# Optimization experiments

Measured on AMD Instinct MI355X. Metric: run time of the kernel, lower is better.

## Reference

```python
import jax, jax.numpy as jnp
import numpy as np

N, E, IN_DIM, OUT_DIM, R = 100000, 1600000, 128, 128, 8


def setup_inputs() -> dict:
    key = jax.random.key(0)
    k = jax.random.split(key, 6)
    scale_rel = np.sqrt(6.0 / (IN_DIM + OUT_DIM))  # xavier_uniform bound
    x = jax.random.normal(k[0], (N, IN_DIM), dtype=jnp.float32)
    edge_index = jax.random.randint(k[1], (2, E), 0, N, dtype=jnp.int64)
    edge_type = jax.random.randint(k[2], (E,), 0, R, dtype=jnp.int64)
    rel_weight = jax.random.uniform(k[3], (R, IN_DIM, OUT_DIM), dtype=jnp.float32,
                                    minval=-scale_rel, maxval=scale_rel)
    w_self = jax.random.uniform(k[4], (IN_DIM, OUT_DIM), dtype=jnp.float32,
                                minval=-scale_rel, maxval=scale_rel)
    b_self = jax.random.normal(k[5], (OUT_DIM,), dtype=jnp.float32) * 0.01
    return {"x": x, "edge_index": edge_index, "edge_type": edge_type,
            "rel_weight": rel_weight, "w_self": w_self, "b_self": b_self}


def reference(x, edge_index, edge_type, rel_weight, w_self, b_self):
    n = x.shape[0]
    src, dst = edge_index[0], edge_index[1]
    # self-loop term: W_self @ h_v + b
    out = x @ w_self + b_self                                  # (N, out)
    # pre-transform every node by every relation, then gather per edge.
    # equivalent to per-relation masked (x[src_r] @ W_r) + scatter_add.
    xw = jnp.einsum('ni,rio->nro', x, rel_weight)               # (N, R, out)
    msg = xw[src, edge_type]                                    # (E, out)
    agg = jax.ops.segment_sum(msg, dst, num_segments=n)         # (N, out)
    deg = jax.ops.segment_sum(jnp.ones(dst.shape[0], x.dtype), dst, num_segments=n)
    deg = jnp.clip(deg, 1.0)[:, None]                           # (N, 1)
    return jax.nn.relu(out + agg / deg)
```

## Files before the change

### kernel.cpp

```cpp
#include <hip/hip_runtime.h>
#include <hip/hip_bf16.h>

typedef __attribute__((ext_vector_type(4))) float f32x4_t;
typedef __attribute__((ext_vector_type(8))) short bf16x8_t;

__device__ __forceinline__ float bf2f(ushort u) {
  return __uint_as_float(((unsigned)u) << 16);
}
__device__ __forceinline__ ushort f2bf(float f) {
  unsigned u = __float_as_uint(f);
  u += 0x7fffu + ((u >> 16) & 1u);
  return (ushort)(u >> 16);
}

__global__ void deg_kernel(const int* __restrict__ dst, int* __restrict__ deg, long E) {
  long i = (long)blockIdx.x * blockDim.x + threadIdx.x;
  long st = (long)gridDim.x * blockDim.x;
  for (; i < E; i += st) atomicAdd(&deg[dst[i]], 1);
}

__global__ __launch_bounds__(256) void scan1(const int* __restrict__ deg, int* __restrict__ starts,
                                             int* __restrict__ bsum, int N) {
  __shared__ int lds[256];
  const int tid = threadIdx.x;
  const int base = blockIdx.x * 1024 + tid * 4;
  int v0 = 0, v1 = 0, v2 = 0, v3 = 0;
  if (base + 3 < N) {
    int4 q = *(const int4*)(deg + base);
    v0 = q.x; v1 = q.y; v2 = q.z; v3 = q.w;
  } else {
    if (base + 0 < N) v0 = deg[base];
    if (base + 1 < N) v1 = deg[base + 1];
    if (base + 2 < N) v2 = deg[base + 2];
    if (base + 3 < N) v3 = deg[base + 3];
  }
  int s = v0 + v1 + v2 + v3;
  lds[tid] = s;
  __syncthreads();
  for (int off = 1; off < 256; off <<= 1) {
    int t = (tid >= off) ? lds[tid - off] : 0;
    __syncthreads();
    lds[tid] += t;
    __syncthreads();
  }
  int p = lds[tid] - s;
  if (tid == 255) bsum[blockIdx.x] = lds[255];
  if (base + 0 < N) starts[base + 0] = p; p += v0;
  if (base + 1 < N) starts[base + 1] = p; p += v1;
  if (base + 2 < N) starts[base + 2] = p; p += v2;
  if (base + 3 < N) starts[base + 3] = p;
}

__global__ void scan2(int* __restrict__ bsum, int nb) {
  if (threadIdx.x == 0 && blockIdx.x == 0) {
    int acc = 0;
    for (int i = 0; i < nb; i++) { int t = bsum[i]; bsum[i] = acc; acc += t; }
  }
}

__global__ void scan3(int* __restrict__ starts, int* __restrict__ cursor,
                      const int* __restrict__ bsum, int N) {
  int i = blockIdx.x * 256 + threadIdx.x;
  if (i < N) {
    int v = starts[i] + bsum[i >> 10];
    starts[i] = v;
    cursor[i] = v;
  }
}

__global__ void fill_csr(const int* __restrict__ src, const int* __restrict__ dst,
                         const int* __restrict__ et, int* __restrict__ cursor,
                         uint* __restrict__ packed, long E) {
  long i = (long)blockIdx.x * blockDim.x + threadIdx.x;
  long st = (long)gridDim.x * blockDim.x;
  for (; i < E; i += st) {
    int pos = atomicAdd(&cursor[dst[i]], 1);
    packed[pos] = ((uint)src[i] << 4) | (uint)et[i];
  }
}

__global__ void build_wT(const float* __restrict__ rel, const float* __restrict__ wself,
                         ushort* __restrict__ wT, int R) {
  int id = blockIdx.x * blockDim.x + threadIdx.x;
  int total = (R + 1) * 128 * 128;
  if (id >= total) return;
  int r = id >> 14;
  int rem = id & 16383;
  int o = rem >> 7;
  int i = rem & 127;
  float v = (r < R) ? rel[((size_t)r << 14) + (i << 7) + o] : wself[(i << 7) + o];
  wT[id] = f2bf(v);
}

__global__ __launch_bounds__(512) void xw_gemm(const float* __restrict__ x,
                                               const ushort* __restrict__ wT,
                                               ushort* __restrict__ xw,
                                               int N, int NR) {
  __shared__ ushort smem[2][16384];

  const int tid = threadIdx.x;
  const int lane = tid & 63;
  const int wave = tid >> 6;
  const int l15 = lane & 15;
  const int l4 = lane >> 4;
  const int nodebase = blockIdx.x * 256 + wave * 32;

  bf16x8_t xf[2][4];
  int nd[2];
#pragma unroll
  for (int g = 0; g < 2; g++) {
    int node = nodebase + g * 16 + l15;
    nd[g] = node;
    int ra = (node < N) ? node : (N - 1);
    const float* xrow = x + (size_t)ra * 128 + l4 * 8;
#pragma unroll
    for (int kk = 0; kk < 4; kk++) {
      float4 v0 = *(const float4*)(xrow + kk * 32);
      float4 v1 = *(const float4*)(xrow + kk * 32 + 4);
      bf16x8_t t;
      t[0] = (short)f2bf(v0.x); t[1] = (short)f2bf(v0.y);
      t[2] = (short)f2bf(v0.z); t[3] = (short)f2bf(v0.w);
      t[4] = (short)f2bf(v1.x); t[5] = (short)f2bf(v1.y);
      t[6] = (short)f2bf(v1.z); t[7] = (short)f2bf(v1.w);
      xf[g][kk] = t;
    }
  }

  {
    bf16x8_t sreg[4];
#pragma unroll
    for (int j = 0; j < 4; j++) {
      int c = tid + j * 512;
      sreg[j] = *(const bf16x8_t*)(wT + c * 8);
    }
#pragma unroll
    for (int j = 0; j < 4; j++) {
      int c = tid + j * 512;
      int o = c >> 4;
      int colb = (c & 15) * 16;
      int byte = o * 256 + (colb ^ ((o & 7) << 4));
      *(bf16x8_t*)((char*)smem[0] + byte) = sreg[j];
    }
  }
  __syncthreads();

  for (int r = 0; r < NR; r++) {
    bf16x8_t sreg[4];
    const bool pf = (r + 1 < NR);
    if (pf) {
      const ushort* wsrc = wT + ((size_t)(r + 1) << 14);
#pragma unroll
      for (int j = 0; j < 4; j++) {
        int c = tid + j * 512;
        sreg[j] = *(const bf16x8_t*)(wsrc + c * 8);
      }
    }

    const char* wbuf = (const char*)smem[r & 1];
#pragma unroll
    for (int nt = 0; nt < 8; nt++) {
      bf16x8_t wf[4];
      const int row = nt * 16 + l15;
      const int swz = (row & 7) << 4;
#pragma unroll
      for (int kk = 0; kk < 4; kk++) {
        int colb = l4 * 16 + kk * 64;
        wf[kk] = *(const bf16x8_t*)(wbuf + row * 256 + (colb ^ swz));
      }
#pragma unroll
      for (int g = 0; g < 2; g++) {
        f32x4_t acc = {0.f, 0.f, 0.f, 0.f};
#pragma unroll
        for (int kk = 0; kk < 4; kk++)
          acc = __builtin_amdgcn_mfma_f32_16x16x32_bf16(wf[kk], xf[g][kk], acc, 0, 0, 0);
        if (nd[g] < N) {
          ushort4 pk;
          pk.x = f2bf(acc[0]); pk.y = f2bf(acc[1]);
          pk.z = f2bf(acc[2]); pk.w = f2bf(acc[3]);
          *(ushort4*)(xw + ((size_t)nd[g] * NR + r) * 128 + nt * 16 + l4 * 4) = pk;
        }
      }
    }

    if (pf) {
#pragma unroll
      for (int j = 0; j < 4; j++) {
        int c = tid + j * 512;
        int o = c >> 4;
        int colb = (c & 15) * 16;
        int byte = o * 256 + (colb ^ ((o & 7) << 4));
        *(bf16x8_t*)((char*)smem[(r + 1) & 1] + byte) = sreg[j];
      }
    }
    __syncthreads();
  }
}

__global__ __launch_bounds__(256) void gather_out(const ushort* __restrict__ xw,
                                                  const uint* __restrict__ packed,
                                                  const int* __restrict__ starts,
                                                  const int* __restrict__ deg,
                                                  const float* __restrict__ b,
                                                  float* __restrict__ out,
                                                  int N, int NR, int R) {
  const int lane = threadIdx.x & 63;
  const int d = blockIdx.x * 4 + (threadIdx.x >> 6);
  if (d >= N) return;
  const int s0 = starts[d];
  const int dg = deg[d];
  const int e1 = s0 + dg;
  float a0 = 0.f, a1 = 0.f;
  int e = s0;
  for (; e + 1 < e1; e += 2) {
    uint r0 = packed[e], r1 = packed[e + 1];
    ushort2 m0 = *(const ushort2*)(xw + ((size_t)(r0 >> 4) * NR + (r0 & 15u)) * 128 + lane * 2);
    ushort2 m1 = *(const ushort2*)(xw + ((size_t)(r1 >> 4) * NR + (r1 & 15u)) * 128 + lane * 2);
    a0 += bf2f(m0.x) + bf2f(m1.x);
    a1 += bf2f(m0.y) + bf2f(m1.y);
  }
  if (e < e1) {
    uint r0 = packed[e];
    ushort2 m0 = *(const ushort2*)(xw + ((size_t)(r0 >> 4) * NR + (r0 & 15u)) * 128 + lane * 2);
    a0 += bf2f(m0.x);
    a1 += bf2f(m0.y);
  }
  float inv = 1.0f / (float)((dg > 1) ? dg : 1);
  ushort2 sf = *(const ushort2*)(xw + ((size_t)d * NR + R) * 128 + lane * 2);
  float2 bb = ((const float2*)b)[lane];
  float* op = out + (size_t)d * 128 + lane * 2;
  op[0] = fmaxf(bf2f(sf.x) + bb.x + a0 * inv, 0.f);
  op[1] = fmaxf(bf2f(sf.y) + bb.y + a1 * inv, 0.f);
}

__global__ void naive_edge(const float* __restrict__ x, const int* __restrict__ src,
                           const int* __restrict__ dst, const int* __restrict__ et,
                           const float* __restrict__ rel, float* __restrict__ agg, long E) {
  const int lane = threadIdx.x & 63;
  long wid = ((long)blockIdx.x * blockDim.x + threadIdx.x) >> 6;
  long nw = ((long)gridDim.x * blockDim.x) >> 6;
  for (long e = wid; e < E; e += nw) {
    int s = src[e];
    int d = dst[e];
    int t = et[e];
    const float* xs = x + (size_t)s * 128;
    const float* w = rel + (size_t)t * 128 * 128;
    float a0 = 0.f, a1 = 0.f;
    for (int i = 0; i < 128; i++) {
      float xv = xs[i];
      a0 += xv * w[i * 128 + lane];
      a1 += xv * w[i * 128 + lane + 64];
    }
    atomicAdd(agg + (size_t)d * 128 + lane, a0);
    atomicAdd(agg + (size_t)d * 128 + lane + 64, a1);
  }
}
__global__ void naive_self(const float* __restrict__ x, const float* __restrict__ ws,
                           const float* __restrict__ b, const int* __restrict__ deg,
                           float* __restrict__ out, int N) {
  int v = blockIdx.x;
  int o = threadIdx.x;
  if (v >= N) return;
  const float* xv = x + (size_t)v * 128;
  float acc = b[o];
  for (int i = 0; i < 128; i++) acc += xv[i] * ws[i * 128 + o];
  float dg = (float)max(deg[v], 1);
  float val = acc + out[(size_t)v * 128 + o] / dg;
  out[(size_t)v * 128 + o] = fmaxf(val, 0.f);
}

extern "C" void kernel_launch(void* const* d_in, const int* in_sizes, int n_in,
                              void* d_out, int out_size, void* d_ws, size_t ws_size,
                              hipStream_t stream) {
  const float* x = (const float*)d_in[0];
  const int* ei = (const int*)d_in[1];
  const int* et = (const int*)d_in[2];
  const float* rel = (const float*)d_in[3];
  const float* wself = (const float*)d_in[4];
  const float* bself = (const float*)d_in[5];
  float* out = (float*)d_out;

  const int N = in_sizes[0] / 128;
  const long E = in_sizes[2];
  const int R = in_sizes[3] / (128 * 128);
  const int NR = R + 1;
  const int* srcp = ei;
  const int* dstp = ei + E;

  size_t off = 0;
  auto alloc = [&](size_t bytes) {
    size_t o = off;
    off += (bytes + 255) & ~(size_t)255;
    return o;
  };
  size_t deg_off = alloc((size_t)N * 4);
  size_t starts_off = alloc((size_t)N * 4);
  size_t cursor_off = alloc((size_t)N * 4);
  size_t bsum_off = alloc(4096);
  size_t wT_off = alloc((size_t)NR * 128 * 128 * 2);
  size_t packed_off = alloc((size_t)E * 4);
  size_t xw_off = alloc((size_t)N * (size_t)NR * 128 * 2);
  const bool main_path = (ws_size >= off);

  int* deg = (int*)((char*)d_ws + deg_off);
  hipMemsetAsync(deg, 0, (size_t)N * 4, stream);
  deg_kernel<<<2048, 256, 0, stream>>>(dstp, deg, E);

  if (main_path) {
    int* starts = (int*)((char*)d_ws + starts_off);
    int* cursor = (int*)((char*)d_ws + cursor_off);
    int* bsum = (int*)((char*)d_ws + bsum_off);
    ushort* wT = (ushort*)((char*)d_ws + wT_off);
    uint* packed = (uint*)((char*)d_ws + packed_off);
    ushort* xw = (ushort*)((char*)d_ws + xw_off);

    const int nb = (N + 1023) / 1024;
    scan1<<<nb, 256, 0, stream>>>(deg, starts, bsum, N);
    scan2<<<1, 64, 0, stream>>>(bsum, nb);
    scan3<<<(N + 255) / 256, 256, 0, stream>>>(starts, cursor, bsum, N);
    fill_csr<<<2048, 256, 0, stream>>>(srcp, dstp, et, cursor, packed, E);
    build_wT<<<(NR * 16384 + 255) / 256, 256, 0, stream>>>(rel, wself, wT, R);
    xw_gemm<<<(N + 255) / 256, 512, 0, stream>>>(x, wT, xw, N, NR);
    gather_out<<<(N + 3) / 4, 256, 0, stream>>>(xw, packed, starts, deg, bself, out, N, NR, R);
  } else {
    hipMemsetAsync(out, 0, (size_t)out_size * 4, stream);
    naive_edge<<<4096, 256, 0, stream>>>(x, srcp, dstp, et, rel, out, E);
    naive_self<<<N, 128, 0, stream>>>(x, wself, bself, deg, out, N);
  }
}
```

Measured before the change: 531.3 us.

## Split CSR build into per-class sub-buckets to spread atomic contention

Each edge is assigned to one of 8 classes based on its index chunk. Degrees, scans and CSR fill cursors are kept per (class, node) pair, which is meant to reduce contention on per-node atomic counters. The single-thread serial block-sum scan is replaced by a 256-thread LDS scan, since the scanned array grows eightfold. In exchange, the gather kernel walks 8 sub-segments per node with extra strided start/degree loads and loses its 2-edge unroll. The scan and memset work also grows with the larger count array.

After: 563.4 us. 1.06x slower.

```diff
diff --git a/kernel.cpp b/kernel.cpp
--- a/kernel.cpp
+++ b/kernel.cpp
@@ -3,6 +3,8 @@
 
 typedef __attribute__((ext_vector_type(4))) float f32x4_t;
 typedef __attribute__((ext_vector_type(8))) short bf16x8_t;
+
+#define NCLS 8
 
 __device__ __forceinline__ float bf2f(ushort u) {
   return __uint_as_float(((unsigned)u) << 16);
@@ -13,26 +15,30 @@
   return (ushort)(u >> 16);
 }
 
-__global__ void deg_kernel(const int* __restrict__ dst, int* __restrict__ deg, long E) {
+__global__ void deg2_kernel(const int* __restrict__ dst, int* __restrict__ deg2,
+                            int N, long E) {
   long i = (long)blockIdx.x * blockDim.x + threadIdx.x;
   long st = (long)gridDim.x * blockDim.x;
-  for (; i < E; i += st) atomicAdd(&deg[dst[i]], 1);
+  for (; i < E; i += st) {
+    int cls = (int)((i >> 8) & (NCLS - 1));
+    atomicAdd(&deg2[(size_t)cls * N + dst[i]], 1);
+  }
 }
 
 __global__ __launch_bounds__(256) void scan1(const int* __restrict__ deg, int* __restrict__ starts,
-                                             int* __restrict__ bsum, int N) {
+                                             int* __restrict__ bsum, int M) {
   __shared__ int lds[256];
   const int tid = threadIdx.x;
   const int base = blockIdx.x * 1024 + tid * 4;
   int v0 = 0, v1 = 0, v2 = 0, v3 = 0;
-  if (base + 3 < N) {
+  if (base + 3 < M) {
     int4 q = *(const int4*)(deg + base);
     v0 = q.x; v1 = q.y; v2 = q.z; v3 = q.w;
   } else {
-    if (base + 0 < N) v0 = deg[base];
-    if (base + 1 < N) v1 = deg[base + 1];
-    if (base + 2 < N) v2 = deg[base + 2];
-    if (base + 3 < N) v3 = deg[base + 3];
+    if (base + 0 < M) v0 = deg[base];
+    if (base + 1 < M) v1 = deg[base + 1];
+    if (base + 2 < M) v2 = deg[base + 2];
+    if (base + 3 < M) v3 = deg[base + 3];
   }
   int s = v0 + v1 + v2 + v3;
   lds[tid] = s;
@@ -45,23 +51,40 @@
   }
   int p = lds[tid] - s;
   if (tid == 255) bsum[blockIdx.x] = lds[255];
-  if (base + 0 < N) starts[base + 0] = p; p += v0;
-  if (base + 1 < N) starts[base + 1] = p; p += v1;
-  if (base + 2 < N) starts[base + 2] = p; p += v2;
-  if (base + 3 < N) starts[base + 3] = p;
-}
-
-__global__ void scan2(int* __restrict__ bsum, int nb) {
-  if (threadIdx.x == 0 && blockIdx.x == 0) {
-    int acc = 0;
-    for (int i = 0; i < nb; i++) { int t = bsum[i]; bsum[i] = acc; acc += t; }
+  if (base + 0 < M) starts[base + 0] = p; p += v0;
+  if (base + 1 < M) starts[base + 1] = p; p += v1;
+  if (base + 2 < M) starts[base + 2] = p; p += v2;
+  if (base + 3 < M) starts[base + 3] = p;
+}
+
+__global__ __launch_bounds__(256) void scan2(int* __restrict__ bsum, int nb) {
+  __shared__ int lds[256];
+  const int tid = threadIdx.x;
+  const int base = tid * 4;
+  int v[4];
+#pragma unroll
+  for (int j = 0; j < 4; j++) v[j] = (base + j < nb) ? bsum[base + j] : 0;
+  int s = v[0] + v[1] + v[2] + v[3];
+  lds[tid] = s;
+  __syncthreads();
+  for (int off = 1; off < 256; off <<= 1) {
+    int t = (tid >= off) ? lds[tid - off] : 0;
+    __syncthreads();
+    lds[tid] += t;
+    __syncthreads();
+  }
+  int p = lds[tid] - s;
+#pragma unroll
+  for (int j = 0; j < 4; j++) {
+    if (base + j < nb) bsum[base + j] = p;
+    p += v[j];
   }
 }
 
 __global__ void scan3(int* __restrict__ starts, int* __restrict__ cursor,
-                      const int* __restrict__ bsum, int N) {
+                      const int* __restrict__ bsum, int M) {
   int i = blockIdx.x * 256 + threadIdx.x;
-  if (i < N) {
+  if (i < M) {
     int v = starts[i] + bsum[i >> 10];
     starts[i] = v;
     cursor[i] = v;
@@ -70,11 +93,12 @@
 
 __global__ void fill_csr(const int* __restrict__ src, const int* __restrict__ dst,
                          const int* __restrict__ et, int* __restrict__ cursor,
-                         uint* __restrict__ packed, long E) {
+                         uint* __restrict__ packed, int N, long E) {
   long i = (long)blockIdx.x * blockDim.x + threadIdx.x;
   long st = (long)gridDim.x * blockDim.x;
   for (; i < E; i += st) {
-    int pos = atomicAdd(&cursor[dst[i]], 1);
+    int cls = (int)((i >> 8) & (NCLS - 1));
+    int pos = atomicAdd(&cursor[(size_t)cls * N + dst[i]], 1);
     packed[pos] = ((uint)src[i] << 4) | (uint)et[i];
   }
 }
@@ -198,31 +222,28 @@
 
 __global__ __launch_bounds__(256) void gather_out(const ushort* __restrict__ xw,
                                                   const uint* __restrict__ packed,
-                                                  const int* __restrict__ starts,
-                                                  const int* __restrict__ deg,
+                                                  const int* __restrict__ starts2,
+                                                  const int* __restrict__ deg2,
                                                   const float* __restrict__ b,
                                                   float* __restrict__ out,
                                                   int N, int NR, int R) {
   const int lane = threadIdx.x & 63;
   const int d = blockIdx.x * 4 + (threadIdx.x >> 6);
   if (d >= N) return;
-  const int s0 = starts[d];
-  const int dg = deg[d];
-  const int e1 = s0 + dg;
   float a0 = 0.f, a1 = 0.f;
-  int e = s0;
-  for (; e + 1 < e1; e += 2) {
-    uint r0 = packed[e], r1 = packed[e + 1];
-    ushort2 m0 = *(const ushort2*)(xw + ((size_t)(r0 >> 4) * NR + (r0 & 15u)) * 128 + lane * 2);
-    ushort2 m1 = *(const ushort2*)(xw + ((size_t)(r1 >> 4) * NR + (r1 & 15u)) * 128 + lane * 2);
-    a0 += bf2f(m0.x) + bf2f(m1.x);
-    a1 += bf2f(m0.y) + bf2f(m1.y);
-  }
-  if (e < e1) {
-    uint r0 = packed[e];
-    ushort2 m0 = *(const ushort2*)(xw + ((size_t)(r0 >> 4) * NR + (r0 & 15u)) * 128 + lane * 2);
-    a0 += bf2f(m0.x);
-    a1 += bf2f(m0.y);
+  int dg = 0;
+#pragma unroll
+  for (int xc = 0; xc < NCLS; xc++) {
+    const int m = xc * N + d;
+    const int s0 = starts2[m];
+    const int len = deg2[m];
+    dg += len;
+    for (int k = 0; k < len; k++) {
+      uint r0 = packed[s0 + k];
+      ushort2 m0 = *(const ushort2*)(xw + ((size_t)(r0 >> 4) * NR + (r0 & 15u)) * 128 + lane * 2);
+      a0 += bf2f(m0.x);
+      a1 += bf2f(m0.y);
+    }
   }
   float inv = 1.0f / (float)((dg > 1) ? dg : 1);
   ushort2 sf = *(const ushort2*)(xw + ((size_t)d * NR + R) * 128 + lane * 2);
@@ -232,6 +253,11 @@
   op[1] = fmaxf(bf2f(sf.y) + bb.y + a1 * inv, 0.f);
 }
 
+__global__ void deg_kernel(const int* __restrict__ dst, int* __restrict__ deg, long E) {
+  long i = (long)blockIdx.x * blockDim.x + threadIdx.x;
+  long st = (long)gridDim.x * blockDim.x;
+  for (; i < E; i += st) atomicAdd(&deg[dst[i]], 1);
+}
 __global__ void naive_edge(const float* __restrict__ x, const int* __restrict__ src,
                            const int* __restrict__ dst, const int* __restrict__ et,
                            const float* __restrict__ rel, float* __restrict__ agg, long E) {
@@ -285,6 +311,7 @@
   const int NR = R + 1;
   const int* srcp = ei;
   const int* dstp = ei + E;
+  const int M = NCLS * N;
 
   size_t off = 0;
   auto alloc = [&](size_t bytes) {
@@ -292,36 +319,39 @@
     off += (bytes + 255) & ~(size_t)255;
     return o;
   };
-  size_t deg_off = alloc((size_t)N * 4);
-  size_t starts_off = alloc((size_t)N * 4);
-  size_t cursor_off = alloc((size_t)N * 4);
+  size_t deg2_off = alloc((size_t)M * 4);
+  size_t starts2_off = alloc((size_t)M * 4);
+  size_t cursor2_off = alloc((size_t)M * 4);
   size_t bsum_off = alloc(4096);
   size_t wT_off = alloc((size_t)NR * 128 * 128 * 2);
   size_t packed_off = alloc((size_t)E * 4);
   size_t xw_off = alloc((size_t)N * (size_t)NR * 128 * 2);
-  const bool main_path = (ws_size >= off);
-
-  int* deg = (int*)((char*)d_ws + deg_off);
-  hipMemsetAsync(deg, 0, (size_t)N * 4, stream);
-  deg_kernel<<<2048, 256, 0, stream>>>(dstp, deg, E);
+  const bool main_path = (ws_size >= off) && (M <= 1024 * 1024);
 
   if (main_path) {
-    int* starts = (int*)((char*)d_ws + starts_off);
-    int* cursor = (int*)((char*)d_ws + cursor_off);
+    int* deg2 = (int*)((char*)d_ws + deg2_off);
+    int* starts2 = (int*)((char*)d_ws + starts2_off);
+    int* cursor2 = (int*)((char*)d_ws + cursor2_off);
     int* bsum = (int*)((char*)d_ws + bsum_off);
     ushort* wT = (ushort*)((char*)d_ws + wT_off);
     uint* packed = (uint*)((char*)d_ws + packed_off);
     ushort* xw = (ushort*)((char*)d_ws + xw_off);
 
-    const int nb = (N + 1023) / 1024;
-    scan1<<<nb, 256, 0, stream>>>(deg, starts, bsum, N);
-    scan2<<<1, 64, 0, stream>>>(bsum, nb);
-    scan3<<<(N + 255) / 256, 256, 0, stream>>>(starts, cursor, bsum, N);
-    fill_csr<<<2048, 256, 0, stream>>>(srcp, dstp, et, cursor, packed, E);
+    hipMemsetAsync(deg2, 0, (size_t)M * 4, stream);
+    deg2_kernel<<<2048, 256, 0, stream>>>(dstp, deg2, N, E);
+
+    const int nb = (M + 1023) / 1024;
+    scan1<<<nb, 256, 0, stream>>>(deg2, starts2, bsum, M);
+    scan2<<<1, 256, 0, stream>>>(bsum, nb);
+    scan3<<<(M + 255) / 256, 256, 0, stream>>>(starts2, cursor2, bsum, M);
+    fill_csr<<<2048, 256, 0, stream>>>(srcp, dstp, et, cursor2, packed, N, E);
     build_wT<<<(NR * 16384 + 255) / 256, 256, 0, stream>>>(rel, wself, wT, R);
     xw_gemm<<<(N + 255) / 256, 512, 0, stream>>>(x, wT, xw, N, NR);
-    gather_out<<<(N + 3) / 4, 256, 0, stream>>>(xw, packed, starts, deg, bself, out, N, NR, R);
+    gather_out<<<(N + 3) / 4, 256, 0, stream>>>(xw, packed, starts2, deg2, bself, out, N, NR, R);
   } else {
+    int* deg = (int*)((char*)d_ws + deg2_off);
+    hipMemsetAsync(deg, 0, (size_t)N * 4, stream);
+    deg_kernel<<<2048, 256, 0, stream>>>(dstp, deg, E);
     hipMemsetAsync(out, 0, (size_t)out_size * 4, stream);
     naive_edge<<<4096, 256, 0, stream>>>(x, srcp, dstp, et, rel, out, E);
     naive_self<<<N, 128, 0, stream>>>(x, wself, bself, deg, out, N);
```
